# Kernel optimization log

Hardware: AMD Instinct MI355X
Metric: run time of the kernel (lower is better)

The kernel has to match this reference:

```python
import jax, jax.numpy as jnp
import numpy as np

B, S, H = 1, 2048, 2048
NH, KVH, D = 32, 8, 64
G = NH // KVH  # num_key_value_groups = 4


def setup_inputs() -> dict:
    key = jax.random.key(0)
    k1, k2, k3 = jax.random.split(key, 3)
    x = jax.random.normal(k1, (B, S, H), dtype=jnp.float32)
    w_qkv = jax.random.normal(k2, ((NH + 2 * KVH) * D, H), dtype=jnp.float32) * 0.02
    w_o = jax.random.normal(k3, (H, NH * D), dtype=jnp.float32) * 0.02
    return {"x": x, "w_qkv": w_qkv, "w_o": w_o}


def _rope_cos_sin(seqlen, dim, dtype):
    inv_freq = 1.0 / (10000.0 ** (jnp.arange(0, dim, 2, dtype=jnp.float32) / dim))
    t = jnp.arange(seqlen, dtype=jnp.float32)
    freqs = jnp.outer(t, inv_freq)  # [S, D/2]
    return jnp.cos(freqs).astype(dtype), jnp.sin(freqs).astype(dtype)


def _apply_rope(x, cos, sin):
    # x: [B,S,h,D]; non-interleaved half rotation (flash-attn RotaryEmbedding)
    d2 = x.shape[-1] // 2
    x1, x2 = x[..., :d2], x[..., d2:]
    c = cos[None, :, None, :]
    s = sin[None, :, None, :]
    return jnp.concatenate([x1 * c - x2 * s, x2 * c + x1 * s], axis=-1)


def reference(x, w_qkv, w_o):
    b, s, _ = x.shape
    qkv = x @ w_qkv.T  # fused QKV proj: [B,S,(NH+2*KVH)*D]
    q, kv = jnp.split(qkv, [NH * D], axis=-1)
    q = q.reshape(b, s, NH, D)
    kv = kv.reshape(b, s, 2, KVH, D)
    cos, sin = _rope_cos_sin(s, D, x.dtype)
    q = _apply_rope(q, cos, sin)
    k = _apply_rope(kv[:, :, 0], cos, sin)
    v = kv[:, :, 1]
    # GQA: group q heads per kv head instead of repeat_interleave (same math)
    qg = q.reshape(b, s, KVH, G, D)
    scale = 1.0 / np.sqrt(D).astype(np.float32)
    scores = jnp.einsum('bskgd,btkd->bkgst', qg, k) * scale  # [B,KVH,G,S,S]
    causal = jnp.tril(jnp.ones((s, s), dtype=bool))
    scores = jnp.where(causal[None, None, None], scores, jnp.asarray(-jnp.inf, scores.dtype))
    p = jax.nn.softmax(scores, axis=-1)
    out = jnp.einsum('bkgst,btkd->bskgd', p, v).reshape(b, s, NH * D)
    return out @ w_o.T
```

## Files before the change

kernel.cpp:

```cpp
#include <hip/hip_runtime.h>


typedef __bf16 bf16_t;
typedef __attribute__((ext_vector_type(8))) __bf16 bf16x8;
typedef __attribute__((ext_vector_type(4))) __bf16 bf16x4;
typedef __attribute__((ext_vector_type(4))) float f32x4;

#define S_LEN 2048
#define H_DIM 2048
#define NHEAD 32
#define KVH 8
#define HD 64
#define QKV_N 3072

#define ENT_STRIDE 8320

__global__ void cast3_kernel(const float* __restrict__ x, const float* __restrict__ wq,
                             const float* __restrict__ wo, bf16_t* __restrict__ xb,
                             bf16_t* __restrict__ wqb, bf16_t* __restrict__ wob) {
  int i = blockIdx.x * blockDim.x + threadIdx.x;
  const int n1 = S_LEN * H_DIM / 4, n2 = QKV_N * H_DIM / 4, n3 = H_DIM * H_DIM / 4;
  const float* src; bf16_t* dst; int j;
  if (i < n1)           { src = x;  dst = xb;  j = i; }
  else if (i < n1 + n2) { src = wq; dst = wqb; j = i - n1; }
  else if (i < n1 + n2 + n3) { src = wo; dst = wob; j = i - n1 - n2; }
  else return;
  float4 v = ((const float4*)src)[j];
  bf16x4 o;
  o.x = (bf16_t)v.x; o.y = (bf16_t)v.y; o.z = (bf16_t)v.z; o.w = (bf16_t)v.w;
  ((bf16x4*)dst)[j] = o;
}

__device__ __forceinline__ void async_copy16(bf16_t* lds_base, const bf16_t* g) {
  __builtin_amdgcn_global_load_lds(
      (const __attribute__((address_space(1))) unsigned int*)g,
      (__attribute__((address_space(3))) unsigned int*)lds_base, 16, 0, 0);
}

#define GBM 128
#define GBN 128
#define GBK 32

template <int EPI>
__global__ __launch_bounds__(512) void gemm512(const bf16_t* __restrict__ A,
                                               const bf16_t* __restrict__ B,
                                               float* __restrict__ C,
                                               bf16_t* __restrict__ qb,
                                               bf16_t* __restrict__ ktp,
                                               bf16_t* __restrict__ vt2,
                                               int M, int N, int K) {
  __shared__ __align__(16) bf16_t As[3][GBM * GBK];
  __shared__ __align__(16) bf16_t Bs[3][GBM * GBK];

  const int tid  = threadIdx.x;
  const int lane = tid & 63;
  const int w    = tid >> 6;
  const int wm   = (w >> 1) * 32;
  const int wn   = (w & 1) * 64;
  const int c    = lane & 15;
  const int quad = lane >> 4;
  const int m0   = blockIdx.y * GBM;
  const int n0   = blockIdx.x * GBN;

  f32x4 acc[2][4] = {};

  const bf16_t* Ab = A + (size_t)m0 * K;
  const bf16_t* Bb = B + (size_t)n0 * K;

  const int srow = tid >> 2;
  const int skch = (tid & 3) ^ ((tid >> 3) & 3);
  const int sbase = (w * 64) * 8;

  auto stage = [&](int buf, int k0) {
    async_copy16(&As[buf][sbase], Ab + (size_t)srow * K + k0 + skch * 8);
    async_copy16(&Bs[buf][sbase], Bb + (size_t)srow * K + k0 + skch * 8);
  };

  auto compute = [&](int buf) {
    bf16x8 af[2], bfr[4];
#pragma unroll
    for (int mt = 0; mt < 2; ++mt) {
      int row = wm + mt * 16 + c;
      int kch = quad ^ ((row >> 1) & 3);
      af[mt] = *(const bf16x8*)&As[buf][(row * 4 + kch) * 8];
    }
#pragma unroll
    for (int nt = 0; nt < 4; ++nt) {
      int rowb = wn + nt * 16 + c;
      int kch = quad ^ ((rowb >> 1) & 3);
      bfr[nt] = *(const bf16x8*)&Bs[buf][(rowb * 4 + kch) * 8];
    }
#pragma unroll
    for (int mt = 0; mt < 2; ++mt)
#pragma unroll
      for (int nt = 0; nt < 4; ++nt)
        acc[mt][nt] = __builtin_amdgcn_mfma_f32_16x16x32_bf16(af[mt], bfr[nt], acc[mt][nt], 0, 0, 0);
  };

  const int NS = K / GBK;
  stage(0, 0);
  stage(1, GBK);
  int sc = 0, sp = 2;
  for (int k = 0; k < NS; ++k) {
    if (k + 1 < NS) {
      asm volatile("s_waitcnt vmcnt(2)" ::: "memory");
    } else {
      asm volatile("s_waitcnt vmcnt(0)" ::: "memory");
    }
    __builtin_amdgcn_s_barrier();
    if (k + 2 < NS) stage(sp, (k + 2) * GBK);
    compute(sc);
    sc = (sc == 2) ? 0 : sc + 1;
    sp = (sp == 2) ? 0 : sp + 1;
  }

  if (EPI == 0) {
#pragma unroll
    for (int mt = 0; mt < 2; ++mt)
#pragma unroll
      for (int nt = 0; nt < 4; ++nt)
#pragma unroll
        for (int reg = 0; reg < 4; ++reg) {
          int row = m0 + wm + mt * 16 + quad * 4 + reg;
          int col = n0 + wn + nt * 16 + c;
          C[(size_t)row * N + col] = acc[mt][nt][reg];
        }
  } else {
    const int colb = n0 + wn;
    if (colb < NHEAD * HD) {
      const int h = colb >> 6;
#pragma unroll
      for (int nt = 0; nt < 2; ++nt) {
        const int i = nt * 16 + c;
        const float invf = __expf(-(float)i * (9.210340371976184f / 32.0f));
#pragma unroll
        for (int mt = 0; mt < 2; ++mt)
#pragma unroll
          for (int reg = 0; reg < 4; ++reg) {
            const int s = m0 + wm + mt * 16 + quad * 4 + reg;
            float sn, cs;
            __sincosf((float)s * invf, &sn, &cs);
            const float x1 = acc[mt][nt][reg], x2 = acc[mt][nt + 2][reg];
            bf16_t* q = qb + (size_t)s * H_DIM + h * HD;
            q[i]      = (bf16_t)((x1 * cs - x2 * sn) * 0.125f);
            q[i + 32] = (bf16_t)((x2 * cs + x1 * sn) * 0.125f);
          }
      }
    } else if (colb < NHEAD * HD + KVH * HD) {
      const int kh = (colb - NHEAD * HD) >> 6;
#pragma unroll
      for (int nt = 0; nt < 2; ++nt) {
        const int i = nt * 16 + c;
        const float invf = __expf(-(float)i * (9.210340371976184f / 32.0f));
#pragma unroll
        for (int mt = 0; mt < 2; ++mt)
#pragma unroll
          for (int reg = 0; reg < 4; ++reg) {
            const int s = m0 + wm + mt * 16 + quad * 4 + reg;
            float sn, cs;
            __sincosf((float)s * invf, &sn, &cs);
            const float x1 = acc[mt][nt][reg], x2 = acc[mt][nt + 2][reg];
            bf16_t* kd = ktp + ((size_t)kh * S_LEN + s) * HD;
            kd[i]      = (bf16_t)(x1 * cs - x2 * sn);
            kd[i + 32] = (bf16_t)(x2 * cs + x1 * sn);
          }
      }
    } else {
      const int kh = (colb - NHEAD * HD - KVH * HD) >> 6;
#pragma unroll
      for (int nt = 0; nt < 4; ++nt) {
        const int d = nt * 16 + c;
#pragma unroll
        for (int mt = 0; mt < 2; ++mt) {
          const int sr = m0 + wm + mt * 16 + quad * 4;
          bf16x4 pv;
#pragma unroll
          for (int reg = 0; reg < 4; ++reg) pv[reg] = (bf16_t)acc[mt][nt][reg];
          *(bf16x4*)&vt2[((size_t)kh * HD + d) * S_LEN + sr] = pv;
        }
      }
    }
  }
}

#define PSTR 72

__global__ __launch_bounds__(256) void flash_split(const bf16_t* __restrict__ qb,
                                                   const bf16_t* __restrict__ kt,
                                                   const bf16_t* __restrict__ vt2,
                                                   float* __restrict__ pbuf,
                                                   bf16_t* __restrict__ attn) {
  __shared__ __align__(16) bf16_t Ks[64 * 64];
  __shared__ __align__(16) bf16_t Vs[64 * 64];
  __shared__ __align__(16) bf16_t Ps[4][32 * PSTR];

  const int tid  = threadIdx.x;
  const int lane = tid & 63;
  const int w    = tid >> 6;
  const int e    = (int)gridDim.x - 1 - (int)blockIdx.x;
  const int kh   = e / 160;
  const int i    = e - kh * 160;

  int qt, t_begin, t_end;
  {
    int T;
    if (i < 16)      { qt = i;                T = (qt >> 1) + 1; t_begin = 0;                 t_end = T; }
    else if (i < 48) { int r = i - 16; qt = 16 + (r >> 1); int ck = r & 1;
                       T = (qt >> 1) + 1; t_begin = (ck * T) >> 1;      t_end = ((ck + 1) * T) >> 1; }
    else if (i < 96) { int r = i - 48; qt = 32 + r / 3;    int ck = r % 3;
                       T = (qt >> 1) + 1; t_begin = (ck * T) / 3;       t_end = ((ck + 1) * T) / 3; }
    else             { int r = i - 96; qt = 48 + (r >> 2); int ck = r & 3;
                       T = (qt >> 1) + 1; t_begin = (ck * T) >> 2;      t_end = ((ck + 1) * T) >> 2; }
  }
  const int T     = (qt >> 1) + 1;
  const int s0    = qt * 32;
  const int h     = kh * 4 + w;
  const int c     = lane & 15;
  const int quad  = lane >> 4;

  bf16x8 qf[2][2];
#pragma unroll
  for (int rf = 0; rf < 2; ++rf)
#pragma unroll
    for (int ks = 0; ks < 2; ++ks)
      qf[rf][ks] = *(const bf16x8*)(qb + (size_t)(s0 + rf * 16 + c) * H_DIM + h * HD + ks * 32 + quad * 8);

  f32x4 acc[2][4] = {};
  float lsum[2] = {0.f, 0.f};

  const bf16_t* kbase = kt + (size_t)kh * S_LEN * HD;
  const bf16_t* vbase = vt2 + (size_t)kh * HD * S_LEN;

  int srow[2], skc[2], sbase[2];
#pragma unroll
  for (int i2 = 0; i2 < 2; ++i2) {
    int chunkbase = i2 * 256 + w * 64;
    int p = chunkbase + lane;
    sbase[i2] = chunkbase * 8;
    srow[i2]  = p >> 3;
    skc[i2]   = (p & 7) ^ (srow[i2] & 7);
  }

  for (int tile = t_begin; tile < t_end; ++tile) {
    const int t0 = tile * 64;
    __syncthreads();
#pragma unroll
    for (int i2 = 0; i2 < 2; ++i2) {
      async_copy16(&Ks[sbase[i2]], kbase + (size_t)(t0 + srow[i2]) * HD + skc[i2] * 8);
      async_copy16(&Vs[sbase[i2]], vbase + (size_t)srow[i2] * S_LEN + t0 + skc[i2] * 8);
    }
    __syncthreads();

    const bool masked = (tile == T - 1);
    int nact = 4;
    if (masked) { nact = ((s0 + 31 - t0) >> 4) + 1; if (nact > 4) nact = 4; }
    const int nkh = (nact + 1) >> 1;

#pragma unroll
    for (int rf = 0; rf < 2; ++rf) {
      for (int kt2 = 0; kt2 < nact; ++kt2) {
        f32x4 st = {};
#pragma unroll
        for (int ks = 0; ks < 2; ++ks) {
          bf16x8 kf = *(const bf16x8*)&Ks[((kt2 * 16 + c) * 8 + ((ks * 4 + quad) ^ (c & 7))) * 8];
          st = __builtin_amdgcn_mfma_f32_16x16x32_bf16(kf, qf[rf][ks], st, 0, 0, 0);
        }
        const int row = s0 + rf * 16 + c;
        bf16x4 pk;
#pragma unroll
        for (int reg = 0; reg < 4; ++reg) {
          const int key = t0 + kt2 * 16 + quad * 4 + reg;
          float p = __expf(st[reg] - 8.0f);
          if (masked && key > row) p = 0.f;
          pk[reg] = (bf16_t)p;
          lsum[rf] += p;
        }
        *(bf16x4*)&Ps[w][(rf * 16 + c) * PSTR + kt2 * 16 + quad * 4] = pk;
      }
      for (int kt2 = nact; kt2 < 2 * nkh; ++kt2) {
        bf16x4 z = {};
        *(bf16x4*)&Ps[w][(rf * 16 + c) * PSTR + kt2 * 16 + quad * 4] = z;
      }
    }

    for (int kh2 = 0; kh2 < nkh; ++kh2) {
      bf16x8 vf[4];
#pragma unroll
      for (int dt = 0; dt < 4; ++dt)
        vf[dt] = *(const bf16x8*)&Vs[((dt * 16 + c) * 8 + ((kh2 * 4 + quad) ^ (c & 7))) * 8];
#pragma unroll
      for (int rf = 0; rf < 2; ++rf) {
        bf16x8 pa = *(const bf16x8*)&Ps[w][(rf * 16 + c) * PSTR + kh2 * 32 + quad * 8];
#pragma unroll
        for (int dt = 0; dt < 4; ++dt)
          acc[rf][dt] = __builtin_amdgcn_mfma_f32_16x16x32_bf16(pa, vf[dt], acc[rf][dt], 0, 0, 0);
      }
    }
  }

#pragma unroll
  for (int rf = 0; rf < 2; ++rf) {
    lsum[rf] += __shfl_xor(lsum[rf], 16);
    lsum[rf] += __shfl_xor(lsum[rf], 32);
  }

  if (i < 16) {
    float* lbuf = (float*)&Ps[w][0];
#pragma unroll
    for (int rf = 0; rf < 2; ++rf) lbuf[rf * 16 + c] = lsum[rf];
    asm volatile("s_waitcnt lgkmcnt(0)" ::: "memory");
#pragma unroll
    for (int rf = 0; rf < 2; ++rf)
#pragma unroll
      for (int reg = 0; reg < 4; ++reg) {
        const float inv = 1.0f / lbuf[rf * 16 + quad * 4 + reg];
        const int row = s0 + rf * 16 + quad * 4 + reg;
#pragma unroll
        for (int dt = 0; dt < 4; ++dt)
          attn[(size_t)row * H_DIM + h * HD + dt * 16 + c] = (bf16_t)(acc[rf][dt][reg] * inv);
      }
  } else {
    float* ent = pbuf + (size_t)e * ENT_STRIDE;
#pragma unroll
    for (int rf = 0; rf < 2; ++rf) {
#pragma unroll
      for (int dt = 0; dt < 4; ++dt)
#pragma unroll
        for (int reg = 0; reg < 4; ++reg)
          ent[w * 2048 + (rf * 16 + quad * 4 + reg) * 64 + dt * 16 + c] = acc[rf][dt][reg];
      ent[8192 + w * 32 + rf * 16 + c] = lsum[rf];
    }
  }
}

__global__ __launch_bounds__(256) void flash_reduce(const float* __restrict__ pbuf,
                                                    bf16_t* __restrict__ attn) {
  const int kh = blockIdx.x / 48;
  const int qt = 16 + (blockIdx.x % 48);
  const int b  = qt >> 4;
  int base;
  if (b == 1)      base = kh * 160 + 16 + (qt - 16) * 2;
  else if (b == 2) base = kh * 160 + 48 + (qt - 32) * 3;
  else             base = kh * 160 + 96 + (qt - 48) * 4;
  const int nch = b + 1;

  const int t   = threadIdx.x;
  const int h2  = t >> 6;
  const int row = (t >> 1) & 31;
  const int dh  = t & 1;

  f32x4 o[8] = {};
  float l = 0.f;
  for (int ci = 0; ci < nch; ++ci) {
    const float* ent = pbuf + (size_t)(base + ci) * ENT_STRIDE;
    const float* p = ent + h2 * 2048 + row * 64 + dh * 32;
#pragma unroll
    for (int j = 0; j < 8; ++j) {
      f32x4 v = ((const f32x4*)p)[j];
      o[j][0] += v[0]; o[j][1] += v[1]; o[j][2] += v[2]; o[j][3] += v[3];
    }
    l += ent[8192 + h2 * 32 + row];
  }
  const float inv = 1.0f / l;
  bf16_t* dst = attn + (size_t)(qt * 32 + row) * H_DIM + (kh * 4 + h2) * 64 + dh * 32;
#pragma unroll
  for (int j = 0; j < 8; ++j) {
    bf16x4 ov;
    ov[0] = (bf16_t)(o[j][0] * inv); ov[1] = (bf16_t)(o[j][1] * inv);
    ov[2] = (bf16_t)(o[j][2] * inv); ov[3] = (bf16_t)(o[j][3] * inv);
    *(bf16x4*)(dst + j * 4) = ov;
  }
}

extern "C" void kernel_launch(void* const* d_in, const int* in_sizes, int n_in,
                              void* d_out, int out_size, void* d_ws, size_t ws_size,
                              hipStream_t stream) {
  const float* x     = (const float*)d_in[0];
  const float* w_qkv = (const float*)d_in[1];
  const float* w_o   = (const float*)d_in[2];
  float* out = (float*)d_out;

  char* ws = (char*)d_ws;
  const size_t OVERLAY = (size_t)1280 * ENT_STRIDE * 4;
  bf16_t* x_bf    = (bf16_t*)ws;
  bf16_t* wqkv_bf = (bf16_t*)(ws + (size_t)S_LEN * H_DIM * 2);
  float*  pbuf    = (float*)ws;
  size_t off = OVERLAY;
  bf16_t* wo_bf   = (bf16_t*)(ws + off); off += (size_t)H_DIM * H_DIM * 2;
  bf16_t* q_bf    = (bf16_t*)(ws + off); off += (size_t)S_LEN * H_DIM * 2;
  bf16_t* k_t     = (bf16_t*)(ws + off); off += (size_t)KVH * S_LEN * HD * 2;
  bf16_t* v_t2    = (bf16_t*)(ws + off); off += (size_t)KVH * S_LEN * HD * 2;
  bf16_t* attn    = (bf16_t*)(ws + off); off += (size_t)S_LEN * H_DIM * 2;

  const int ntot = (S_LEN * H_DIM + QKV_N * H_DIM + H_DIM * H_DIM) / 4;
  cast3_kernel<<<(ntot + 255) / 256, 256, 0, stream>>>(x, w_qkv, w_o, x_bf, wqkv_bf, wo_bf);

  gemm512<1><<<dim3(QKV_N / GBN, S_LEN / GBM), 512, 0, stream>>>(
      x_bf, wqkv_bf, nullptr, q_bf, k_t, v_t2, S_LEN, QKV_N, H_DIM);

  flash_split<<<1280, 256, 0, stream>>>(q_bf, k_t, v_t2, pbuf, attn);
  flash_reduce<<<384, 256, 0, stream>>>(pbuf, attn);

  gemm512<0><<<dim3(H_DIM / GBN, S_LEN / GBM), 512, 0, stream>>>(
      attn, wo_bf, out, nullptr, nullptr, nullptr, S_LEN, H_DIM, H_DIM);
}
```

Before: 233.3 us.

## Split K across wave groups in GEMM with 64x64 warp tiles and LDS reduction

The 128x128 GEMM block now uses a K-step of 64, with two groups of four waves. Each group covers half of the K chunk with a 64x64 warp tile, which raises MFMA work per LDS fragment load. The two groups' partial accumulators are combined through LDS before the epilogue, and the pipeline moves from three buffers to two with a full vmcnt(0) wait each iteration. The goal is better operand reuse and fewer loop iterations. The cost is more accumulator registers, a reduction step, and less overlap between memory and compute.

```diff
diff --git a/kernel.cpp b/kernel.cpp
--- a/kernel.cpp
+++ b/kernel.cpp
@@ -39,144 +39,161 @@
 
 #define GBM 128
 #define GBN 128
-#define GBK 32
 
 template <int EPI>
-__global__ __launch_bounds__(512) void gemm512(const bf16_t* __restrict__ A,
-                                               const bf16_t* __restrict__ B,
-                                               float* __restrict__ C,
-                                               bf16_t* __restrict__ qb,
-                                               bf16_t* __restrict__ ktp,
-                                               bf16_t* __restrict__ vt2,
-                                               int M, int N, int K) {
-  __shared__ __align__(16) bf16_t As[3][GBM * GBK];
-  __shared__ __align__(16) bf16_t Bs[3][GBM * GBK];
+__global__ __launch_bounds__(512, 4) void gemm_sk(const bf16_t* __restrict__ A,
+                                                  const bf16_t* __restrict__ B,
+                                                  float* __restrict__ C,
+                                                  bf16_t* __restrict__ qb,
+                                                  bf16_t* __restrict__ ktp,
+                                                  bf16_t* __restrict__ vt2,
+                                                  int M, int N, int K) {
+  __shared__ __align__(16) bf16_t As[2][GBM * 64];
+  __shared__ __align__(16) bf16_t Bs[2][GBM * 64];
 
   const int tid  = threadIdx.x;
   const int lane = tid & 63;
   const int w    = tid >> 6;
-  const int wm   = (w >> 1) * 32;
-  const int wn   = (w & 1) * 64;
+  const int wq   = w & 3;
+  const int gw   = w >> 2;
+  const int wm   = (wq >> 1) * 64;
+  const int wn   = (wq & 1) * 64;
   const int c    = lane & 15;
   const int quad = lane >> 4;
   const int m0   = blockIdx.y * GBM;
   const int n0   = blockIdx.x * GBN;
 
-  f32x4 acc[2][4] = {};
+  f32x4 acc[4][4] = {};
 
   const bf16_t* Ab = A + (size_t)m0 * K;
   const bf16_t* Bb = B + (size_t)n0 * K;
 
-  const int srow = tid >> 2;
-  const int skch = (tid & 3) ^ ((tid >> 3) & 3);
-  const int sbase = (w * 64) * 8;
+  int srow[2], skc[2], sb[2];
+#pragma unroll
+  for (int i = 0; i < 2; ++i) {
+    int p = i * 512 + tid;
+    srow[i] = p >> 3;
+    skc[i]  = (p & 7) ^ (srow[i] & 7);
+    sb[i]   = (i * 512 + w * 64) * 8;
+  }
 
   auto stage = [&](int buf, int k0) {
-    async_copy16(&As[buf][sbase], Ab + (size_t)srow * K + k0 + skch * 8);
-    async_copy16(&Bs[buf][sbase], Bb + (size_t)srow * K + k0 + skch * 8);
+#pragma unroll
+    for (int i = 0; i < 2; ++i) {
+      async_copy16(&As[buf][sb[i]], Ab + (size_t)srow[i] * K + k0 + skc[i] * 8);
+      async_copy16(&Bs[buf][sb[i]], Bb + (size_t)srow[i] * K + k0 + skc[i] * 8);
+    }
   };
 
   auto compute = [&](int buf) {
-    bf16x8 af[2], bfr[4];
-#pragma unroll
-    for (int mt = 0; mt < 2; ++mt) {
+    bf16x8 af[4], bfr[4];
+#pragma unroll
+    for (int mt = 0; mt < 4; ++mt) {
       int row = wm + mt * 16 + c;
-      int kch = quad ^ ((row >> 1) & 3);
-      af[mt] = *(const bf16x8*)&As[buf][(row * 4 + kch) * 8];
+      af[mt] = *(const bf16x8*)&As[buf][(row * 8 + ((gw * 4 + quad) ^ (row & 7))) * 8];
     }
 #pragma unroll
     for (int nt = 0; nt < 4; ++nt) {
       int rowb = wn + nt * 16 + c;
-      int kch = quad ^ ((rowb >> 1) & 3);
-      bfr[nt] = *(const bf16x8*)&Bs[buf][(rowb * 4 + kch) * 8];
-    }
-#pragma unroll
-    for (int mt = 0; mt < 2; ++mt)
+      bfr[nt] = *(const bf16x8*)&Bs[buf][(rowb * 8 + ((gw * 4 + quad) ^ (rowb & 7))) * 8];
+    }
+#pragma unroll
+    for (int mt = 0; mt < 4; ++mt)
 #pragma unroll
       for (int nt = 0; nt < 4; ++nt)
         acc[mt][nt] = __builtin_amdgcn_mfma_f32_16x16x32_bf16(af[mt], bfr[nt], acc[mt][nt], 0, 0, 0);
   };
 
-  const int NS = K / GBK;
+  const int NI = K >> 6;
   stage(0, 0);
-  stage(1, GBK);
-  int sc = 0, sp = 2;
-  for (int k = 0; k < NS; ++k) {
-    if (k + 1 < NS) {
-      asm volatile("s_waitcnt vmcnt(2)" ::: "memory");
+  int buf = 0;
+  for (int it = 0; it < NI; ++it) {
+    asm volatile("s_waitcnt vmcnt(0)" ::: "memory");
+    __builtin_amdgcn_s_barrier();
+    if (it + 1 < NI) stage(buf ^ 1, (it + 1) << 6);
+    compute(buf);
+    buf ^= 1;
+  }
+
+  __syncthreads();
+  float* xch = (float*)&As[0][0];
+  if (gw == 1) {
+#pragma unroll
+    for (int t16 = 0; t16 < 16; ++t16)
+      *(f32x4*)&xch[wq * 4096 + (t16 * 64 + lane) * 4] = acc[t16 >> 2][t16 & 3];
+  }
+  __syncthreads();
+  if (gw == 0) {
+#pragma unroll
+    for (int t16 = 0; t16 < 16; ++t16) {
+      f32x4 o = *(const f32x4*)&xch[wq * 4096 + (t16 * 64 + lane) * 4];
+      acc[t16 >> 2][t16 & 3] += o;
+    }
+
+    if (EPI == 0) {
+#pragma unroll
+      for (int mt = 0; mt < 4; ++mt)
+#pragma unroll
+        for (int nt = 0; nt < 4; ++nt)
+#pragma unroll
+          for (int reg = 0; reg < 4; ++reg) {
+            int row = m0 + wm + mt * 16 + quad * 4 + reg;
+            int col = n0 + wn + nt * 16 + c;
+            C[(size_t)row * N + col] = acc[mt][nt][reg];
+          }
     } else {
-      asm volatile("s_waitcnt vmcnt(0)" ::: "memory");
-    }
-    __builtin_amdgcn_s_barrier();
-    if (k + 2 < NS) stage(sp, (k + 2) * GBK);
-    compute(sc);
-    sc = (sc == 2) ? 0 : sc + 1;
-    sp = (sp == 2) ? 0 : sp + 1;
-  }
-
-  if (EPI == 0) {
-#pragma unroll
-    for (int mt = 0; mt < 2; ++mt)
-#pragma unroll
-      for (int nt = 0; nt < 4; ++nt)
-#pragma unroll
-        for (int reg = 0; reg < 4; ++reg) {
-          int row = m0 + wm + mt * 16 + quad * 4 + reg;
-          int col = n0 + wn + nt * 16 + c;
-          C[(size_t)row * N + col] = acc[mt][nt][reg];
+      const int colb = n0 + wn;
+      if (colb < NHEAD * HD) {
+        const int h = colb >> 6;
+#pragma unroll
+        for (int nt = 0; nt < 2; ++nt) {
+          const int i = nt * 16 + c;
+          const float invf = __expf(-(float)i * (9.210340371976184f / 32.0f));
+#pragma unroll
+          for (int mt = 0; mt < 4; ++mt)
+#pragma unroll
+            for (int reg = 0; reg < 4; ++reg) {
+              const int s = m0 + wm + mt * 16 + quad * 4 + reg;
+              float sn, cs;
+              __sincosf((float)s * invf, &sn, &cs);
+              const float x1 = acc[mt][nt][reg], x2 = acc[mt][nt + 2][reg];
+              bf16_t* q = qb + (size_t)s * H_DIM + h * HD;
+              q[i]      = (bf16_t)((x1 * cs - x2 * sn) * 0.125f);
+              q[i + 32] = (bf16_t)((x2 * cs + x1 * sn) * 0.125f);
+            }
         }
-  } else {
-    const int colb = n0 + wn;
-    if (colb < NHEAD * HD) {
-      const int h = colb >> 6;
-#pragma unroll
-      for (int nt = 0; nt < 2; ++nt) {
-        const int i = nt * 16 + c;
-        const float invf = __expf(-(float)i * (9.210340371976184f / 32.0f));
-#pragma unroll
-        for (int mt = 0; mt < 2; ++mt)
-#pragma unroll
-          for (int reg = 0; reg < 4; ++reg) {
-            const int s = m0 + wm + mt * 16 + quad * 4 + reg;
-            float sn, cs;
-            __sincosf((float)s * invf, &sn, &cs);
-            const float x1 = acc[mt][nt][reg], x2 = acc[mt][nt + 2][reg];
-            bf16_t* q = qb + (size_t)s * H_DIM + h * HD;
-            q[i]      = (bf16_t)((x1 * cs - x2 * sn) * 0.125f);
-            q[i + 32] = (bf16_t)((x2 * cs + x1 * sn) * 0.125f);
+      } else if (colb < NHEAD * HD + KVH * HD) {
+        const int kh = (colb - NHEAD * HD) >> 6;
+#pragma unroll
+        for (int nt = 0; nt < 2; ++nt) {
+          const int i = nt * 16 + c;
+          const float invf = __expf(-(float)i * (9.210340371976184f / 32.0f));
+#pragma unroll
+          for (int mt = 0; mt < 4; ++mt)
+#pragma unroll
+            for (int reg = 0; reg < 4; ++reg) {
+              const int s = m0 + wm + mt * 16 + quad * 4 + reg;
+              float sn, cs;
+              __sincosf((float)s * invf, &sn, &cs);
+              const float x1 = acc[mt][nt][reg], x2 = acc[mt][nt + 2][reg];
+              bf16_t* kd = ktp + ((size_t)kh * S_LEN + s) * HD;
+              kd[i]      = (bf16_t)(x1 * cs - x2 * sn);
+              kd[i + 32] = (bf16_t)(x2 * cs + x1 * sn);
+            }
+        }
+      } else {
+        const int kh = (colb - NHEAD * HD - KVH * HD) >> 6;
+#pragma unroll
+        for (int nt = 0; nt < 4; ++nt) {
+          const int d = nt * 16 + c;
+#pragma unroll
+          for (int mt = 0; mt < 4; ++mt) {
+            const int sr = m0 + wm + mt * 16 + quad * 4;
+            bf16x4 pv;
+#pragma unroll
+            for (int reg = 0; reg < 4; ++reg) pv[reg] = (bf16_t)acc[mt][nt][reg];
+            *(bf16x4*)&vt2[((size_t)kh * HD + d) * S_LEN + sr] = pv;
           }
-      }
-    } else if (colb < NHEAD * HD + KVH * HD) {
-      const int kh = (colb - NHEAD * HD) >> 6;
-#pragma unroll
-      for (int nt = 0; nt < 2; ++nt) {
-        const int i = nt * 16 + c;
-        const float invf = __expf(-(float)i * (9.210340371976184f / 32.0f));
-#pragma unroll
-        for (int mt = 0; mt < 2; ++mt)
-#pragma unroll
-          for (int reg = 0; reg < 4; ++reg) {
-            const int s = m0 + wm + mt * 16 + quad * 4 + reg;
-            float sn, cs;
-            __sincosf((float)s * invf, &sn, &cs);
-            const float x1 = acc[mt][nt][reg], x2 = acc[mt][nt + 2][reg];
-            bf16_t* kd = ktp + ((size_t)kh * S_LEN + s) * HD;
-            kd[i]      = (bf16_t)(x1 * cs - x2 * sn);
-            kd[i + 32] = (bf16_t)(x2 * cs + x1 * sn);
-          }
-      }
-    } else {
-      const int kh = (colb - NHEAD * HD - KVH * HD) >> 6;
-#pragma unroll
-      for (int nt = 0; nt < 4; ++nt) {
-        const int d = nt * 16 + c;
-#pragma unroll
-        for (int mt = 0; mt < 2; ++mt) {
-          const int sr = m0 + wm + mt * 16 + quad * 4;
-          bf16x4 pv;
-#pragma unroll
-          for (int reg = 0; reg < 4; ++reg) pv[reg] = (bf16_t)acc[mt][nt][reg];
-          *(bf16x4*)&vt2[((size_t)kh * HD + d) * S_LEN + sr] = pv;
         }
       }
     }
@@ -395,12 +412,12 @@
   const int ntot = (S_LEN * H_DIM + QKV_N * H_DIM + H_DIM * H_DIM) / 4;
   cast3_kernel<<<(ntot + 255) / 256, 256, 0, stream>>>(x, w_qkv, w_o, x_bf, wqkv_bf, wo_bf);
 
-  gemm512<1><<<dim3(QKV_N / GBN, S_LEN / GBM), 512, 0, stream>>>(
+  gemm_sk<1><<<dim3(QKV_N / GBN, S_LEN / GBM), 512, 0, stream>>>(
       x_bf, wqkv_bf, nullptr, q_bf, k_t, v_t2, S_LEN, QKV_N, H_DIM);
 
   flash_split<<<1280, 256, 0, stream>>>(q_bf, k_t, v_t2, pbuf, attn);
   flash_reduce<<<384, 256, 0, stream>>>(pbuf, attn);
 
-  gemm512<0><<<dim3(H_DIM / GBN, S_LEN / GBM), 512, 0, stream>>>(
+  gemm_sk<0><<<dim3(H_DIM / GBN, S_LEN / GBM), 512, 0, stream>>>(
       attn, wo_bf, out, nullptr, nullptr, nullptr, S_LEN, H_DIM, H_DIM);
 }
```

New measurement: 216.9 us. -7.0%, faster.
